# Optimization experiments

Hardware: AMD Instinct MI355X
Metric: run time of the kernel (lower is better)

The kernel has to match this reference:

```python
import jax, jax.numpy as jnp
import numpy as np

DELTA_COEFF = 1.0
CLAMP_MIN = 1e-3  # hardcoded in original clamp(min=0.001)


def setup_inputs() -> dict:
    key = jax.random.key(0)
    k1, k2, k3 = jax.random.split(key, 3)
    B, N, F_in, F_out = 2, 1024, 128, 64
    x = jax.random.normal(k1, (B, N, F_in), dtype=jnp.float32)
    adj = jax.random.uniform(k2, (B, N, N), dtype=jnp.float32)
    weight = jax.random.normal(k3, (F_in, F_out), dtype=jnp.float32) * (1.0 / np.sqrt(F_in))
    bias = jnp.zeros((F_out,), dtype=jnp.float32)
    return {"x": x, "adj": adj, "weight": weight, "bias": bias}


def reference(x, adj, weight, bias):
    # x: [B,N,F_in], adj: [B,N,N]
    x = x @ weight  # [B,N,F_out]
    B, N, _ = adj.shape
    # pairwise L1 distance: [B,N,N]
    abs_diff = jnp.sum(jnp.abs(x[:, :, None, :] - x[:, None, :, :]), axis=-1)
    mod_adj = adj / jnp.maximum(abs_diff, CLAMP_MIN)
    deg = jnp.sum(mod_adj, axis=-1)  # [B,N]
    # Laplacian L = D - A~ ; then I - delta * L
    lap = jnp.zeros_like(mod_adj).at[:, jnp.arange(N), jnp.arange(N)].set(deg) - mod_adj
    mod = jnp.eye(N, dtype=x.dtype) - DELTA_COEFF * lap
    out = jnp.matmul(mod, x) + bias
    return out
```

## Files before the change

### kernel.cpp

```cpp
#include <hip/hip_runtime.h>
#include <hip/hip_fp16.h>


#define JS 16
#define HSTR 72

__device__ __forceinline__ void fma4(float4& a, float s, const float4 v) {
    a.x += s * v.x; a.y += s * v.y; a.z += s * v.z; a.w += s * v.w;
}

__global__ __launch_bounds__(256) void gemm_xw(const float* __restrict__ x,
                                               const float* __restrict__ w,
                                               float* __restrict__ xw,
                                               __half* __restrict__ xwh) {
    __shared__ float ws_[128 * 64];
    __shared__ float xs[8 * 132];
    const int tid = threadIdx.x;
    const int r0  = blockIdx.x * 8;

#pragma unroll
    for (int e = tid; e < 2048; e += 256)
        ((float4*)ws_)[e] = ((const float4*)w)[e];
    {
        int row = tid >> 5, c = tid & 31;
        float4 v = *(const float4*)&x[(size_t)(r0 + row) * 128 + c * 4];
        *(float4*)&xs[row * 132 + c * 4] = v;
    }
    __syncthreads();

    const int rl = tid >> 5;
    const int fg = tid & 31;
    float2 acc = {0.f, 0.f};
#pragma unroll 8
    for (int k = 0; k < 128; ++k) {
        float xv = xs[rl * 132 + k];
        float2 wv = *(const float2*)&ws_[k * 64 + 2 * fg];
        acc.x += xv * wv.x; acc.y += xv * wv.y;
    }
    size_t o = (size_t)(r0 + rl) * 64 + 2 * fg;
    *(float2*)&xw[o] = acc;
    *(__half2*)&xwh[o] = __floats2half2_rn(acc.x, acc.y);
}

template <bool ATOMIC>
__global__ __launch_bounds__(256) void fused_gtv(const float* __restrict__ xw,
                                                 const __half* __restrict__ xwh,
                                                 const float* __restrict__ adj,
                                                 float* __restrict__ pout,
                                                 float* __restrict__ pdeg) {
    __shared__ __half xih[32 * HSTR];
    __shared__ __half xjh[64 * HSTR];
    __shared__ float  xjf[64 * 64];
    __shared__ float  wt[64 * 36];

    const int tid = threadIdx.x;
    const int bx  = blockIdx.x;
    const int js  = bx & 15;
    const int it  = (bx >> 4) & 31;
    const int b   = bx >> 9;
    const int i0  = it * 32;
    const int j0  = js * 64;

    const float*  xwb = xw  + (size_t)b * 65536;
    const __half* xhb = xwh + (size_t)b * 65536;
    const float*  adjb = adj + (size_t)b * 1048576;

    const int ty = tid >> 5;
    const int tx = tid & 31;

    float2 av[4];
#pragma unroll
    for (int r = 0; r < 4; ++r)
        av[r] = *(const float2*)&adjb[(size_t)(i0 + 4 * ty + r) * 1024 + j0 + 2 * tx];

    {
        int row = tid >> 3, c = tid & 7;
        float4 v = *(const float4*)&xhb[(i0 + row) * 64 + c * 8];
        *(float4*)&xih[row * HSTR + c * 8] = v;
    }
#pragma unroll
    for (int e = tid; e < 512; e += 256) {
        int row = e >> 3, c = e & 7;
        float4 v = *(const float4*)&xhb[(j0 + row) * 64 + c * 8];
        *(float4*)&xjh[row * HSTR + c * 8] = v;
    }
#pragma unroll
    for (int e = tid; e < 1024; e += 256) {
        int row = e >> 4, c = e & 15;
        float4 v = *(const float4*)&xwb[(j0 + row) * 64 + c * 4];
        *(float4*)&xjf[row * 64 + c * 4] = v;
    }
    __syncthreads();

    __half2 acc[4][2];
#pragma unroll
    for (int r = 0; r < 4; ++r)
#pragma unroll
        for (int q = 0; q < 2; ++q) acc[r][q] = __floats2half2_rn(0.f, 0.f);

#pragma unroll
    for (int c = 0; c < 8; ++c) {
        float4 a[4], bb[2];
#pragma unroll
        for (int r = 0; r < 4; ++r)
            a[r] = *(const float4*)&xih[(4 * ty + r) * HSTR + c * 8];
#pragma unroll
        for (int q = 0; q < 2; ++q)
            bb[q] = *(const float4*)&xjh[(2 * tx + q) * HSTR + c * 8];
#pragma unroll
        for (int r = 0; r < 4; ++r) {
            const __half2* pa = (const __half2*)&a[r];
#pragma unroll
            for (int q = 0; q < 2; ++q) {
                const __half2* pb = (const __half2*)&bb[q];
#pragma unroll
                for (int m = 0; m < 4; ++m)
                    acc[r][q] = __hadd2(acc[r][q], __habs2(__hsub2(pa[m], pb[m])));
            }
        }
    }

#pragma unroll
    for (int q = 0; q < 2; ++q) {
        float4 wq;
        float* wp = &wq.x;
#pragma unroll
        for (int r = 0; r < 4; ++r) {
            float d = __low2float(acc[r][q]) + __high2float(acc[r][q]);
            wp[r] = (&av[r].x)[q] / fmaxf(d, 1e-3f);
        }
        *(float4*)&wt[(2 * tx + q) * 36 + 4 * ty] = wq;
    }
    __syncthreads();

    const int i2 = tid >> 4;
    const int fg = tid & 15;
    float4 acc2[2] = {{0,0,0,0},{0,0,0,0}};
    float  dg[2]   = {0.f, 0.f};
#pragma unroll 8
    for (int j = 0; j < 64; ++j) {
        float2 wv = *(const float2*)&wt[j * 36 + 2 * i2];
        float4 xv = *(const float4*)&xjf[j * 64 + 4 * fg];
        fma4(acc2[0], wv.x, xv);
        fma4(acc2[1], wv.y, xv);
        dg[0] += wv.x; dg[1] += wv.y;
    }

    if (ATOMIC) {
#pragma unroll
        for (int r = 0; r < 2; ++r) {
            float* op = pout + ((size_t)b * 1024 + i0 + 2 * i2 + r) * 64 + 4 * fg;
            float* ap = &acc2[r].x;
#pragma unroll
            for (int m = 0; m < 4; ++m) atomicAdd(&op[m], ap[m]);
            if (fg == 0) atomicAdd(&pdeg[b * 1024 + i0 + 2 * i2 + r], dg[r]);
        }
    } else {
        const size_t slot = (size_t)(js * 2 + b) * 65536;
#pragma unroll
        for (int r = 0; r < 2; ++r) {
            *(float4*)&pout[slot + (i0 + 2 * i2 + r) * 64 + 4 * fg] = acc2[r];
            if (fg == 0) pdeg[(js * 2 + b) * 1024 + i0 + 2 * i2 + r] = dg[r];
        }
    }
}

template <bool ATOMIC>
__global__ __launch_bounds__(256) void finish_gtv(const float* __restrict__ xw,
                                                  const float* __restrict__ part,
                                                  const float* __restrict__ pdeg,
                                                  const float* __restrict__ bias,
                                                  float* __restrict__ out) {
    int idx = blockIdx.x * 256 + threadIdx.x;
    int f = idx & 63;
    int r = idx >> 6;
    int b = r >> 10;
    if (ATOMIC) {
        out[idx] = out[idx] + (1.f - pdeg[r]) * xw[idx] + bias[f];
    } else {
        int loc = idx & 65535;
        int n   = r & 1023;
        float s = 0.f, dgs = 0.f;
#pragma unroll
        for (int js = 0; js < JS; ++js) {
            s   += part[(size_t)(js * 2 + b) * 65536 + loc];
            dgs += pdeg[(js * 2 + b) * 1024 + n];
        }
        out[idx] = s + (1.f - dgs) * xw[idx] + bias[f];
    }
}

extern "C" void kernel_launch(void* const* d_in, const int* in_sizes, int n_in,
                              void* d_out, int out_size, void* d_ws, size_t ws_size,
                              hipStream_t stream) {
    const float* x    = (const float*)d_in[0];
    const float* adj  = (const float*)d_in[1];
    const float* w    = (const float*)d_in[2];
    const float* bias = (const float*)d_in[3];
    float* out = (float*)d_out;

    char* wsb = (char*)d_ws;
    float*  xw   = (float*)wsb;
    __half* xwh  = (__half*)(wsb + 512 * 1024);
    float*  pdeg = (float*)(wsb + 768 * 1024);
    float*  part = (float*)(wsb + 896 * 1024);
    const size_t NEED = 896 * 1024 + (size_t)32 * 65536 * 4;

    gemm_xw<<<256, 256, 0, stream>>>(x, w, xw, xwh);

    if (ws_size >= NEED) {
        fused_gtv<false><<<1024, 256, 0, stream>>>(xw, xwh, adj, part, pdeg);
        finish_gtv<false><<<512, 256, 0, stream>>>(xw, part, pdeg, bias, out);
    } else {
        hipMemsetAsync(out, 0, 2 * 1024 * 64 * sizeof(float), stream);
        hipMemsetAsync(pdeg, 0, 2 * 1024 * sizeof(float), stream);
        fused_gtv<true><<<1024, 256, 0, stream>>>(xw, xwh, adj, out, pdeg);
        finish_gtv<true><<<512, 256, 0, stream>>>(xw, nullptr, pdeg, bias, out);
    }
}
```

Before: 88.27 us.

## Use fp16 MFMA for weighted aggregation with transposed xw and shuffle-reduced degree

The second-stage product of the weight tile with x_j now runs on 16x16x32 fp16 MFMA instructions instead of scalar fp32 FMAs. To feed it, gemm_xw also writes a transposed fp16 copy of xw, and the weights are stored as fp16 in shared memory. Row degrees are now computed with warp shuffles. The diagonal term is zeroed explicitly, which is mathematically neutral. Rounding the weights and features to fp16 lowers accuracy, and fp32 shared-memory traffic is reduced.

Measured after the change: 85.08 us. -3.6%, faster.

```diff
diff --git a/kernel.cpp b/kernel.cpp
--- a/kernel.cpp
+++ b/kernel.cpp
@@ -5,16 +5,17 @@
 #define JS 16
 #define HSTR 72
 
-__device__ __forceinline__ void fma4(float4& a, float s, const float4 v) {
-    a.x += s * v.x; a.y += s * v.y; a.z += s * v.z; a.w += s * v.w;
-}
+typedef _Float16 half8_t __attribute__((ext_vector_type(8)));
+typedef float    f32x4_t __attribute__((ext_vector_type(4)));
 
 __global__ __launch_bounds__(256) void gemm_xw(const float* __restrict__ x,
                                                const float* __restrict__ w,
                                                float* __restrict__ xw,
-                                               __half* __restrict__ xwh) {
+                                               __half* __restrict__ xwh,
+                                               __half* __restrict__ xwt) {
     __shared__ float ws_[128 * 64];
     __shared__ float xs[8 * 132];
+    __shared__ __half ts[8 * 64];
     const int tid = threadIdx.x;
     const int r0  = blockIdx.x * 8;
 
@@ -39,19 +40,32 @@
     }
     size_t o = (size_t)(r0 + rl) * 64 + 2 * fg;
     *(float2*)&xw[o] = acc;
-    *(__half2*)&xwh[o] = __floats2half2_rn(acc.x, acc.y);
+    __half2 h2 = __floats2half2_rn(acc.x, acc.y);
+    *(__half2*)&xwh[o] = h2;
+    *(__half2*)&ts[rl * 64 + 2 * fg] = h2;
+    __syncthreads();
+
+    if (tid < 64) {
+        const int f = tid;
+        const int b = r0 >> 10;
+        const int n0 = r0 & 1023;
+        __half hv[8];
+#pragma unroll
+        for (int r = 0; r < 8; ++r) hv[r] = ts[r * 64 + f];
+        *(half8_t*)&xwt[((size_t)(b * 64 + f)) * 1024 + n0] = *(half8_t*)hv;
+    }
 }
 
 template <bool ATOMIC>
-__global__ __launch_bounds__(256) void fused_gtv(const float* __restrict__ xw,
-                                                 const __half* __restrict__ xwh,
+__global__ __launch_bounds__(256) void fused_gtv(const __half* __restrict__ xwh,
+                                                 const __half* __restrict__ xwt,
                                                  const float* __restrict__ adj,
                                                  float* __restrict__ pout,
                                                  float* __restrict__ pdeg) {
     __shared__ __half xih[32 * HSTR];
     __shared__ __half xjh[64 * HSTR];
-    __shared__ float  xjf[64 * 64];
-    __shared__ float  wt[64 * 36];
+    __shared__ __half xjt[64 * HSTR];
+    __shared__ __half wt[32 * HSTR];
 
     const int tid = threadIdx.x;
     const int bx  = blockIdx.x;
@@ -61,8 +75,8 @@
     const int i0  = it * 32;
     const int j0  = js * 64;
 
-    const float*  xwb = xw  + (size_t)b * 65536;
     const __half* xhb = xwh + (size_t)b * 65536;
+    const __half* xtb = xwt + (size_t)b * 65536;
     const float*  adjb = adj + (size_t)b * 1048576;
 
     const int ty = tid >> 5;
@@ -83,12 +97,8 @@
         int row = e >> 3, c = e & 7;
         float4 v = *(const float4*)&xhb[(j0 + row) * 64 + c * 8];
         *(float4*)&xjh[row * HSTR + c * 8] = v;
-    }
-#pragma unroll
-    for (int e = tid; e < 1024; e += 256) {
-        int row = e >> 4, c = e & 15;
-        float4 v = *(const float4*)&xwb[(j0 + row) * 64 + c * 4];
-        *(float4*)&xjf[row * 64 + c * 4] = v;
+        float4 t = *(const float4*)&xtb[row * 1024 + j0 + c * 8];
+        *(float4*)&xjt[row * HSTR + c * 8] = t;
     }
     __syncthreads();
 
@@ -120,47 +130,68 @@
         }
     }
 
-#pragma unroll
-    for (int q = 0; q < 2; ++q) {
-        float4 wq;
-        float* wp = &wq.x;
-#pragma unroll
-        for (int r = 0; r < 4; ++r) {
+    float dsum[4];
+#pragma unroll
+    for (int r = 0; r < 4; ++r) {
+        const int gi = i0 + 4 * ty + r;
+        float wv[2];
+#pragma unroll
+        for (int q = 0; q < 2; ++q) {
+            const int gj = j0 + 2 * tx + q;
             float d = __low2float(acc[r][q]) + __high2float(acc[r][q]);
-            wp[r] = (&av[r].x)[q] / fmaxf(d, 1e-3f);
-        }
-        *(float4*)&wt[(2 * tx + q) * 36 + 4 * ty] = wq;
-    }
-    __syncthreads();
-
-    const int i2 = tid >> 4;
-    const int fg = tid & 15;
-    float4 acc2[2] = {{0,0,0,0},{0,0,0,0}};
-    float  dg[2]   = {0.f, 0.f};
-#pragma unroll 8
-    for (int j = 0; j < 64; ++j) {
-        float2 wv = *(const float2*)&wt[j * 36 + 2 * i2];
-        float4 xv = *(const float4*)&xjf[j * 64 + 4 * fg];
-        fma4(acc2[0], wv.x, xv);
-        fma4(acc2[1], wv.y, xv);
-        dg[0] += wv.x; dg[1] += wv.y;
+            float v = (&av[r].x)[q] / fmaxf(d, 1e-3f);
+            wv[q] = (gi == gj) ? 0.f : v;
+        }
+        *(__half2*)&wt[(4 * ty + r) * HSTR + 2 * tx] = __floats2half2_rn(wv[0], wv[1]);
+        dsum[r] = wv[0] + wv[1];
+    }
+#pragma unroll
+    for (int r = 0; r < 4; ++r) {
+#pragma unroll
+        for (int m = 1; m < 32; m <<= 1)
+            dsum[r] += __shfl_xor(dsum[r], m, 32);
+    }
+    if (tx == 0) {
+#pragma unroll
+        for (int r = 0; r < 4; ++r) {
+            if (ATOMIC) atomicAdd(&pdeg[b * 1024 + i0 + 4 * ty + r], dsum[r]);
+            else pdeg[(js * 2 + b) * 1024 + i0 + 4 * ty + r] = dsum[r];
+        }
+    }
+    __syncthreads();
+
+    const int wv   = tid >> 6;
+    const int lane = tid & 63;
+    const int quad = lane >> 4;
+    const int l15  = lane & 15;
+    const int m16  = wv & 1;
+    const int npair = wv >> 1;
+
+    f32x4_t c0 = {0.f, 0.f, 0.f, 0.f};
+    f32x4_t c1 = {0.f, 0.f, 0.f, 0.f};
+#pragma unroll
+    for (int s = 0; s < 2; ++s) {
+        half8_t af = *(half8_t*)&wt[(m16 * 16 + l15) * HSTR + s * 32 + quad * 8];
+        half8_t b0 = *(half8_t*)&xjt[((npair * 2 + 0) * 16 + l15) * HSTR + s * 32 + quad * 8];
+        half8_t b1 = *(half8_t*)&xjt[((npair * 2 + 1) * 16 + l15) * HSTR + s * 32 + quad * 8];
+        c0 = __builtin_amdgcn_mfma_f32_16x16x32_f16(af, b0, c0, 0, 0, 0);
+        c1 = __builtin_amdgcn_mfma_f32_16x16x32_f16(af, b1, c1, 0, 0, 0);
     }
 
     if (ATOMIC) {
 #pragma unroll
-        for (int r = 0; r < 2; ++r) {
-            float* op = pout + ((size_t)b * 1024 + i0 + 2 * i2 + r) * 64 + 4 * fg;
-            float* ap = &acc2[r].x;
-#pragma unroll
-            for (int m = 0; m < 4; ++m) atomicAdd(&op[m], ap[m]);
-            if (fg == 0) atomicAdd(&pdeg[b * 1024 + i0 + 2 * i2 + r], dg[r]);
+        for (int r = 0; r < 4; ++r) {
+            int row = m16 * 16 + quad * 4 + r;
+            atomicAdd(&pout[((size_t)b * 1024 + i0 + row) * 64 + (npair * 2) * 16 + l15], c0[r]);
+            atomicAdd(&pout[((size_t)b * 1024 + i0 + row) * 64 + (npair * 2 + 1) * 16 + l15], c1[r]);
         }
     } else {
         const size_t slot = (size_t)(js * 2 + b) * 65536;
 #pragma unroll
-        for (int r = 0; r < 2; ++r) {
-            *(float4*)&pout[slot + (i0 + 2 * i2 + r) * 64 + 4 * fg] = acc2[r];
-            if (fg == 0) pdeg[(js * 2 + b) * 1024 + i0 + 2 * i2 + r] = dg[r];
+        for (int r = 0; r < 4; ++r) {
+            int row = m16 * 16 + quad * 4 + r;
+            pout[slot + (i0 + row) * 64 + (npair * 2) * 16 + l15] = c0[r];
+            pout[slot + (i0 + row) * 64 + (npair * 2 + 1) * 16 + l15] = c1[r];
         }
     }
 }
@@ -202,19 +233,20 @@
     char* wsb = (char*)d_ws;
     float*  xw   = (float*)wsb;
     __half* xwh  = (__half*)(wsb + 512 * 1024);
-    float*  pdeg = (float*)(wsb + 768 * 1024);
-    float*  part = (float*)(wsb + 896 * 1024);
-    const size_t NEED = 896 * 1024 + (size_t)32 * 65536 * 4;
-
-    gemm_xw<<<256, 256, 0, stream>>>(x, w, xw, xwh);
+    __half* xwt  = (__half*)(wsb + 768 * 1024);
+    float*  pdeg = (float*)(wsb + 1024 * 1024);
+    float*  part = (float*)(wsb + 1152 * 1024);
+    const size_t NEED = 1152 * 1024 + (size_t)32 * 65536 * 4;
+
+    gemm_xw<<<256, 256, 0, stream>>>(x, w, xw, xwh, xwt);
 
     if (ws_size >= NEED) {
-        fused_gtv<false><<<1024, 256, 0, stream>>>(xw, xwh, adj, part, pdeg);
+        fused_gtv<false><<<1024, 256, 0, stream>>>(xwh, xwt, adj, part, pdeg);
         finish_gtv<false><<<512, 256, 0, stream>>>(xw, part, pdeg, bias, out);
     } else {
         hipMemsetAsync(out, 0, 2 * 1024 * 64 * sizeof(float), stream);
         hipMemsetAsync(pdeg, 0, 2 * 1024 * sizeof(float), stream);
-        fused_gtv<true><<<1024, 256, 0, stream>>>(xw, xwh, adj, out, pdeg);
+        fused_gtv<true><<<1024, 256, 0, stream>>>(xwh, xwt, adj, out, pdeg);
         finish_gtv<true><<<512, 256, 0, stream>>>(xw, nullptr, pdeg, bias, out);
     }
 }
```
